# Kernel optimization log

Hardware: AMD Instinct MI355X
Metric: run time of the kernel (lower is better)

## Reference

```python
import jax, jax.numpy as jnp
import numpy as np

N_NODES = 100000
N_EDGES = 1600000
N_GRAPHS = 512
NEG_SLOPE = 0.2  # PyG GATConv default


def setup_inputs() -> dict:
    key = jax.random.key(0)
    ks = jax.random.split(key, 12)
    x = jax.random.normal(ks[0], (N_NODES, 75), dtype=jnp.float32)
    edge_index = jax.random.randint(ks[1], (2, N_EDGES), 0, N_NODES, dtype=jnp.int64 if jax.config.jax_enable_x64 else jnp.int32)
    batch = jnp.sort(jax.random.randint(ks[2], (N_NODES,), 0, N_GRAPHS, dtype=jnp.int32))
    s = lambda k, shp, fan: jax.random.normal(k, shp, dtype=jnp.float32) * (1.0 / np.sqrt(fan))
    return {
        "x": x, "edge_index": edge_index, "batch": batch,
        "W1": s(ks[3], (75, 64), 75),           # conv1: heads=8, out=8
        "att_src1": s(ks[4], (8, 8), 8),
        "att_dst1": s(ks[5], (8, 8), 8),
        "bias1": jnp.zeros((64,), jnp.float32),
        "W2": s(ks[6], (64, 128), 64),          # conv2: heads=1, out=128
        "att_src2": s(ks[7], (1, 128), 128),
        "att_dst2": s(ks[8], (1, 128), 128),
        "bias2": jnp.zeros((128,), jnp.float32),
        "Wg": s(ks[9], (128, 1), 128),
        "bg": jnp.zeros((1,), jnp.float32),
    }


def _gat_conv(x, src, dst, W, att_src, att_dst, bias, heads, out_ch):
    # x: [N, F_in]; edges src->dst (self-loops already included)
    n = x.shape[0]
    h = (x @ W).reshape(n, heads, out_ch)            # [N, H, C]
    a_src = (h * att_src).sum(-1)                    # [N, H]
    a_dst = (h * att_dst).sum(-1)                    # [N, H]
    e = a_src[src] + a_dst[dst]                      # [E, H]
    e = jax.nn.leaky_relu(e, NEG_SLOPE)
    # segment softmax over incoming edges of each dst node
    emax = jax.ops.segment_max(e, dst, num_segments=n)      # [N, H]
    ee = jnp.exp(e - emax[dst])
    denom = jax.ops.segment_sum(ee, dst, num_segments=n)    # [N, H]
    alpha = ee / denom[dst]                                  # [E, H]
    msg = h[src] * alpha[:, :, None]                          # [E, H, C]
    out = jax.ops.segment_sum(msg, dst, num_segments=n)      # [N, H, C]
    return out.reshape(n, heads * out_ch) + bias


def reference(x, edge_index, batch, W1, att_src1, att_dst1, bias1,
              W2, att_src2, att_dst2, bias2, Wg, bg):
    n = x.shape[0]
    # PyG GATConv adds self-loops by default
    loops = jnp.arange(n, dtype=edge_index.dtype)
    src = jnp.concatenate([edge_index[0], loops])
    dst = jnp.concatenate([edge_index[1], loops])
    # eval mode: dropout is identity
    x2 = jax.nn.elu(_gat_conv(x, src, dst, W1, att_src1, att_dst1, bias1, heads=8, out_ch=8))
    x4 = _gat_conv(x2, src, dst, W2, att_src2, att_dst2, bias2, heads=1, out_ch=128)
    y = jax.ops.segment_sum(x4, batch, num_segments=N_GRAPHS)  # global_add_pool
    return y @ Wg + bg  # [N_GRAPHS, 1]
```

## Files before the change

kernel.cpp:

```cpp
#include <hip/hip_runtime.h>
#include <hip/hip_bf16.h>
#include <math.h>

#define N_NODES 100000
#define N_EDGES 1600000
#define ET (N_EDGES + N_NODES)
#define N_GRAPHS 512
#define NEG_SLOPE 0.2f
#define G2_BLOCKS 1280

#define BSH 7
#define NDB 128
#define NBUCK ((N_NODES + NDB - 1) / NDB)
#define BCAP 2560
#define ABLK 512
#define CHUNK ((ET + ABLK - 1) / ABLK)
#define F1_OFF (ABLK + 3)
#define PRE_GRID (F1_OFF + 1536)

__device__ __forceinline__ void atomAddF(float* p, float v) { unsafeAtomicAdd(p, v); }
__device__ __forceinline__ float lrelu(float v) { return v >= 0.f ? v : NEG_SLOPE * v; }

__device__ __forceinline__ unsigned short f2bf(float f) {
    unsigned int u = __float_as_uint(f);
    u += 0x7FFFu + ((u >> 16) & 1u);
    return (unsigned short)(u >> 16);
}
__device__ __forceinline__ float bf2f(unsigned short s) { return __uint_as_float(((unsigned int)s) << 16); }
__device__ __forceinline__ float bflo(unsigned int p) { return __uint_as_float(p << 16); }
__device__ __forceinline__ float bfhi(unsigned int p) { return __uint_as_float(p & 0xFFFF0000u); }

__global__ __launch_bounds__(256) void k_pre(
    const int* __restrict__ ei, uint2* __restrict__ gbuf, int* __restrict__ bcur,
    const float* __restrict__ x, const float* __restrict__ W1,
    const float* __restrict__ as1, const float* __restrict__ ad1,
    const float* __restrict__ W2, const float* __restrict__ as2,
    const float* __restrict__ ad2, const float* __restrict__ Wg,
    const float* __restrict__ b2, const float* __restrict__ bg,
    unsigned short* __restrict__ h1p, unsigned short* __restrict__ a1sh,
    float* __restrict__ a1d, float* __restrict__ wv, float* __restrict__ out)
{
    __shared__ __align__(16) char smem[CHUNK * 8 + NBUCK * 16 + 1024];
    const int t = threadIdx.x;
    const int blk = blockIdx.x;

    if (blk >= ABLK && blk < F1_OFF) {
        const int bb = blk - ABLK;
        if (bb == 0) {
            if (t < 192) {
                int c = t & 63, which = t >> 6;
                const float* v = (which == 0) ? Wg : ((which == 1) ? as2 : ad2);
                float s = 0.f;
                #pragma unroll
                for (int k = 0; k < 128; ++k) s += W2[c * 128 + k] * v[k];
                wv[which * 64 + c] = s;
            } else if (t == 192) {
                float s = 0.f;
                #pragma unroll
                for (int k = 0; k < 128; ++k) s += b2[k] * Wg[k];
                wv[192] = s;
            }
        } else {
            int i = (bb - 1) * 256 + t;
            if (i < N_GRAPHS) out[i] = bg[0];
        }
        return;
    }

    if (blk >= F1_OFF) {
        float (*xs)[76] = (float (*)[76])smem;
        const int g = t >> 6;
        const int c = t & 63;
        const int vb = blk - F1_OFF;
        const int fstride = PRE_GRID - F1_OFF;
        for (int nb = vb; nb < N_NODES / 4; nb += fstride) {
            const int n = nb * 4 + g;
            const float* xr = x + (long)n * 75;
            xs[g][c] = xr[c];
            if (c < 11) xs[g][64 + c] = xr[64 + c];
            __syncthreads();
            float h = 0.f;
            #pragma unroll
            for (int k = 0; k < 75; ++k) h += xs[g][k] * W1[k * 64 + c];
            h1p[(long)n * 64 + c] = f2bf(h);
            const int head = c >> 3, lane = c & 7;
            float vs = h * as1[c];
            float vd = h * ad1[c];
            #pragma unroll
            for (int off = 1; off < 8; off <<= 1) {
                vs += __shfl_xor(vs, off, 64);
                vd += __shfl_xor(vd, off, 64);
            }
            if (lane == 0) { a1sh[n * 8 + head] = f2bf(vs); a1d[n * 8 + head] = vd; }
            __syncthreads();
        }
        return;
    }

    uint2* pairs = (uint2*)smem;
    int* hist  = (int*)(smem + CHUNK * 8);
    int* excl  = hist + NBUCK;
    int* gbase = excl + NBUCK;
    int* cnt2  = gbase + NBUCK;
    int* red   = cnt2 + NBUCK;
    const long e0 = (long)blk * CHUNK;
    const int  n  = (int)((e0 + CHUNK <= ET) ? CHUNK : (ET - e0));
    for (int i = t; i < NBUCK; i += 256) { hist[i] = 0; cnt2[i] = 0; }
    __syncthreads();
    for (int i = t; i < n; i += 256) {
        long e = e0 + i;
        int dst = (e < N_EDGES) ? ei[N_EDGES + e] : (int)(e - N_EDGES);
        atomicAdd(&hist[dst >> BSH], 1);
    }
    __syncthreads();
    {
        int lk[4]; int s = 0;
        #pragma unroll
        for (int k = 0; k < 4; ++k) {
            int idx = t * 4 + k;
            int v = (idx < NBUCK) ? hist[idx] : 0;
            lk[k] = s; s += v;
        }
        red[t] = s;
        __syncthreads();
        for (int off = 1; off < 256; off <<= 1) {
            int a = (t >= off) ? red[t - off] : 0;
            __syncthreads();
            red[t] += a;
            __syncthreads();
        }
        int p = red[t] - s;
        #pragma unroll
        for (int k = 0; k < 4; ++k) {
            int idx = t * 4 + k;
            if (idx < NBUCK) excl[idx] = p + lk[k];
        }
    }
    __syncthreads();
    for (int i = t; i < n; i += 256) {
        long e = e0 + i;
        int src, dst;
        if (e < N_EDGES) { src = ei[e]; dst = ei[N_EDGES + e]; }
        else             { src = dst = (int)(e - N_EDGES); }
        int b = dst >> BSH;
        int pos = excl[b] + atomicAdd(&cnt2[b], 1);
        pairs[pos] = make_uint2((unsigned)src, (unsigned)dst);
    }
    __syncthreads();
    for (int b = t; b < NBUCK; b += 256)
        gbase[b] = hist[b] ? atomicAdd(&bcur[b], hist[b]) : 0;
    __syncthreads();
    for (int i = t; i < n; i += 256) {
        uint2 pr = pairs[i];
        int b = (int)(pr.y >> BSH);
        gbuf[(long)b * BCAP + gbase[b] + (i - excl[b])] = pr;
    }
}

__global__ __launch_bounds__(512) void k_gat1(
    const uint2* __restrict__ gbuf, const int* __restrict__ bcur,
    int* __restrict__ rowptr, int* __restrict__ ecol,
    const unsigned short* __restrict__ a1sh, const float* __restrict__ a1d,
    const unsigned short* __restrict__ h1p, const float* __restrict__ bias1,
    const float* __restrict__ wv,
    float2* __restrict__ sg2, float* __restrict__ a2dv)
{
    __shared__ int lds_ecol[BCAP];
    __shared__ int hist[NDB], excl[NDB + 1], cnt2[NDB];
    __shared__ int red[512];
    const int t = threadIdx.x;
    const int b = blockIdx.x;
    const int d0 = b << BSH;
    const int nloc = (N_NODES - d0 < NDB) ? (N_NODES - d0) : NDB;
    const int cnt = bcur[b];

    int partial = 0;
    for (int i = t; i < b; i += 512) partial += bcur[i];
    red[t] = partial;
    __syncthreads();
    for (int off = 256; off > 0; off >>= 1) {
        if (t < off) red[t] += red[t + off];
        __syncthreads();
    }
    const int base = red[0];
    __syncthreads();

    if (t < NDB) { hist[t] = 0; cnt2[t] = 0; }
    __syncthreads();
    const uint2* eb = gbuf + (long)b * BCAP;
    for (int i = t; i < cnt; i += 512) atomicAdd(&hist[(int)eb[i].y - d0], 1);
    __syncthreads();
    {
        int v = (t < NDB) ? hist[t] : 0;
        if (t < NDB) red[t] = v;
        __syncthreads();
        for (int off = 1; off < NDB; off <<= 1) {
            int a = (t < NDB && t >= off) ? red[t - off] : 0;
            __syncthreads();
            if (t < NDB) red[t] += a;
            __syncthreads();
        }
        if (t < nloc) excl[t] = red[t] - v;
        if (t == 0) excl[nloc] = cnt;
    }
    __syncthreads();
    if (t < nloc) rowptr[d0 + t] = base + excl[t];
    if (b == NBUCK - 1 && t == 0) rowptr[N_NODES] = base + cnt;
    for (int i = t; i < cnt; i += 512) {
        uint2 pr = eb[i];
        int dl = (int)pr.y - d0;
        int slot = excl[dl] + atomicAdd(&cnt2[dl], 1);
        lds_ecol[slot] = (int)pr.x;
    }
    __syncthreads();
    for (int i = t; i < cnt; i += 512) ecol[base + i] = lds_ecol[i];

    const int wave = t >> 6;
    const int lane = t & 63;
    const int g = lane >> 3;
    const int l = lane & 7;
    for (int di = wave; di < nloc; di += 8) {
        const int dst = d0 + di;
        const int beg = excl[di], end = excl[di + 1];
        const float adh = a1d[(long)dst * 8 + l];

        float acc[8] = {0.f,0.f,0.f,0.f,0.f,0.f,0.f,0.f};
        float den = 0.f;

        int j = beg + g;
        bool v = (j < end);
        int s = v ? lds_ecol[j] : 0;
        unsigned short ab = a1sh[(long)s * 8 + l];
        uint4 pv = *(const uint4*)(h1p + (long)s * 64 + l * 8);

        for (int j0 = beg; j0 < end; j0 += 8) {
            int jn = j + 8;
            bool vn = (jn < end);
            int sn = vn ? lds_ecol[jn] : 0;
            unsigned short abn = a1sh[(long)sn * 8 + l];
            uint4 pvn = *(const uint4*)(h1p + (long)sn * 64 + l * 8);
            float ee = v ? __expf(lrelu(bf2f(ab) + adh)) : 0.f;
            den += ee;
            acc[0] += ee * bflo(pv.x); acc[1] += ee * bfhi(pv.x);
            acc[2] += ee * bflo(pv.y); acc[3] += ee * bfhi(pv.y);
            acc[4] += ee * bflo(pv.z); acc[5] += ee * bfhi(pv.z);
            acc[6] += ee * bflo(pv.w); acc[7] += ee * bfhi(pv.w);
            j = jn; v = vn; s = sn; ab = abn; pv = pvn;
        }
        #pragma unroll
        for (int off = 8; off <= 32; off <<= 1) {
            den += __shfl_xor(den, off, 64);
            #pragma unroll
            for (int k = 0; k < 8; ++k) acc[k] += __shfl_xor(acc[k], off, 64);
        }

        if (g == 0) {
            const float inv = 1.f / den;
            float pg = 0.f, ps = 0.f, pd = 0.f;
            #pragma unroll
            for (int k = 0; k < 8; ++k) {
                float vv = acc[k] * inv + bias1[l * 8 + k];
                vv = vv > 0.f ? vv : (__expf(vv) - 1.f);
                pg += vv * wv[l * 8 + k];
                ps += vv * wv[64 + l * 8 + k];
                pd += vv * wv[128 + l * 8 + k];
            }
            #pragma unroll
            for (int off = 1; off < 8; off <<= 1) {
                pg += __shfl_xor(pg, off, 64);
                ps += __shfl_xor(ps, off, 64);
                pd += __shfl_xor(pd, off, 64);
            }
            if (l == 0) { sg2[dst] = make_float2(ps, pg); a2dv[dst] = pd; }
        }
    }
}

__global__ __launch_bounds__(256) void k_gat2(
    const int* __restrict__ rowptr, const int* __restrict__ ecol,
    const float2* __restrict__ sg2, const float* __restrict__ a2dv,
    const float* __restrict__ wv, const int* __restrict__ batch,
    float* __restrict__ out)
{
    const int lane = threadIdx.x & 63;
    const int sl = lane & 15;
    const int sgid = ((blockIdx.x * 256 + threadIdx.x) >> 4);
    const int NS = G2_BLOCKS * 16;
    const int per = (N_NODES + NS - 1) / NS;
    const int n0 = sgid * per;
    const int n1 = min(n0 + per, N_NODES);
    const float bc = wv[192];

    float accg = 0.f;
    int curg = -1;
    for (int n = n0; n < n1; ++n) {
        const int beg = rowptr[n], end = rowptr[n + 1];
        const float adv = a2dv[n];
        float num = 0.f, den = 0.f;
        for (int j = beg + sl; j < end; j += 16) {
            int s = ecol[j];
            float2 v = sg2[s];
            float ee = __expf(lrelu(v.x + adv));
            den += ee;
            num += ee * v.y;
        }
        #pragma unroll
        for (int off = 1; off < 16; off <<= 1) {
            den += __shfl_xor(den, off, 64);
            num += __shfl_xor(num, off, 64);
        }
        if (sl == 0) {
            int gr = batch[n];
            if (gr != curg) {
                if (curg >= 0) atomAddF(out + curg, accg);
                curg = gr; accg = 0.f;
            }
            accg += num / den + bc;
        }
    }
    if (sl == 0 && curg >= 0) atomAddF(out + curg, accg);
}

extern "C" void kernel_launch(void* const* d_in, const int* in_sizes, int n_in,
                              void* d_out, int out_size, void* d_ws, size_t ws_size,
                              hipStream_t stream) {
    (void)in_sizes; (void)n_in; (void)out_size; (void)ws_size;
    const float* x     = (const float*)d_in[0];
    const int*   ei    = (const int*)d_in[1];
    const int*   batch = (const int*)d_in[2];
    const float* W1    = (const float*)d_in[3];
    const float* as1   = (const float*)d_in[4];
    const float* ad1   = (const float*)d_in[5];
    const float* b1    = (const float*)d_in[6];
    const float* W2    = (const float*)d_in[7];
    const float* as2   = (const float*)d_in[8];
    const float* ad2   = (const float*)d_in[9];
    const float* b2    = (const float*)d_in[10];
    const float* Wg    = (const float*)d_in[11];
    const float* bg    = (const float*)d_in[12];
    float* out = (float*)d_out;

    const long N = N_NODES;
    char* p = (char*)d_ws;
    int* rowptr = (int*)p;              p += (N + 4)        * sizeof(int);
    int* bcur   = (int*)p;              p += 1024           * sizeof(int);
    int* ecol   = (int*)p;              p += (long)ET       * sizeof(int);
    uint2* gbuf = (uint2*)p;            p += (long)NBUCK * BCAP * sizeof(uint2);
    unsigned short* h1p  = (unsigned short*)p; p += N * 64  * sizeof(unsigned short);
    unsigned short* a1sh = (unsigned short*)p; p += N * 8   * sizeof(unsigned short);
    float* a1d  = (float*)p;            p += N * 8          * sizeof(float);
    float2* sg2 = (float2*)p;           p += N              * sizeof(float2);
    float* a2dv = (float*)p;            p += N              * sizeof(float);
    float* wv   = (float*)p;            p += 256            * sizeof(float);

    hipMemsetAsync(bcur, 0, NBUCK * sizeof(int), stream);
    k_pre <<<PRE_GRID, 256, 0, stream>>>(ei, gbuf, bcur, x, W1, as1, ad1,
                                         W2, as2, ad2, Wg, b2, bg,
                                         h1p, a1sh, a1d, wv, out);
    k_gat1<<<NBUCK, 512, 0, stream>>>(gbuf, bcur, rowptr, ecol,
                                      a1sh, a1d, h1p, b1, wv, sg2, a2dv);
    k_gat2<<<G2_BLOCKS, 256, 0, stream>>>(rowptr, ecol, sg2, a2dv, wv, batch, out);
}
```

Before: 284.9 us.

## Assign one 8-lane group per destination node in GAT layer 1 with triple-buffered gathers

```diff
diff --git a/kernel.cpp b/kernel.cpp
--- a/kernel.cpp
+++ b/kernel.cpp
@@ -165,14 +165,15 @@
     const float* __restrict__ wv,
     float2* __restrict__ sg2, float* __restrict__ a2dv)
 {
-    __shared__ int lds_ecol[BCAP];
+    __shared__ int lds_src[BCAP];
     __shared__ int hist[NDB], excl[NDB + 1], cnt2[NDB];
     __shared__ int red[512];
     const int t = threadIdx.x;
     const int b = blockIdx.x;
     const int d0 = b << BSH;
     const int nloc = (N_NODES - d0 < NDB) ? (N_NODES - d0) : NDB;
-    const int cnt = bcur[b];
+    int cntr = bcur[b];
+    const int cnt = cntr < BCAP ? cntr : BCAP;
 
     int partial = 0;
     for (int i = t; i < b; i += 512) partial += bcur[i];
@@ -210,69 +211,86 @@
         uint2 pr = eb[i];
         int dl = (int)pr.y - d0;
         int slot = excl[dl] + atomicAdd(&cnt2[dl], 1);
-        lds_ecol[slot] = (int)pr.x;
-    }
-    __syncthreads();
-    for (int i = t; i < cnt; i += 512) ecol[base + i] = lds_ecol[i];
-
-    const int wave = t >> 6;
-    const int lane = t & 63;
-    const int g = lane >> 3;
-    const int l = lane & 7;
-    for (int di = wave; di < nloc; di += 8) {
-        const int dst = d0 + di;
-        const int beg = excl[di], end = excl[di + 1];
+        lds_src[slot] = (int)pr.x;
+    }
+    __syncthreads();
+    for (int i = t; i < cnt; i += 512) ecol[base + i] = lds_src[i];
+
+    const int l = t & 7;
+    const int gid = t >> 3;
+    for (int dl = gid; dl < nloc; dl += 64) {
+        const int dst = d0 + dl;
+        const int beg = excl[dl];
+        const int dgl = excl[dl + 1] - beg;
         const float adh = a1d[(long)dst * 8 + l];
 
         float acc[8] = {0.f,0.f,0.f,0.f,0.f,0.f,0.f,0.f};
         float den = 0.f;
 
-        int j = beg + g;
-        bool v = (j < end);
-        int s = v ? lds_ecol[j] : 0;
-        unsigned short ab = a1sh[(long)s * 8 + l];
-        uint4 pv = *(const uint4*)(h1p + (long)s * 64 + l * 8);
-
-        for (int j0 = beg; j0 < end; j0 += 8) {
-            int jn = j + 8;
-            bool vn = (jn < end);
-            int sn = vn ? lds_ecol[jn] : 0;
-            unsigned short abn = a1sh[(long)sn * 8 + l];
-            uint4 pvn = *(const uint4*)(h1p + (long)sn * 64 + l * 8);
-            float ee = v ? __expf(lrelu(bf2f(ab) + adh)) : 0.f;
+        bool v0 = true, v1 = 1 < dgl, v2 = 2 < dgl;
+        int s0 = lds_src[beg];
+        int s1 = v1 ? lds_src[beg + 1] : 0;
+        int s2 = v2 ? lds_src[beg + 2] : 0;
+        unsigned short ab0 = a1sh[(long)s0 * 8 + l];
+        unsigned short ab1 = a1sh[(long)s1 * 8 + l];
+        unsigned short ab2 = a1sh[(long)s2 * 8 + l];
+        uint4 pv0 = *(const uint4*)(h1p + (long)s0 * 64 + l * 8);
+        uint4 pv1 = *(const uint4*)(h1p + (long)s1 * 64 + l * 8);
+        uint4 pv2 = *(const uint4*)(h1p + (long)s2 * 64 + l * 8);
+
+        for (int j = 0; j < dgl; j += 3) {
+            float ee;
+            ee = v0 ? __expf(lrelu(bf2f(ab0) + adh)) : 0.f;
             den += ee;
-            acc[0] += ee * bflo(pv.x); acc[1] += ee * bfhi(pv.x);
-            acc[2] += ee * bflo(pv.y); acc[3] += ee * bfhi(pv.y);
-            acc[4] += ee * bflo(pv.z); acc[5] += ee * bfhi(pv.z);
-            acc[6] += ee * bflo(pv.w); acc[7] += ee * bfhi(pv.w);
-            j = jn; v = vn; s = sn; ab = abn; pv = pvn;
-        }
-        #pragma unroll
-        for (int off = 8; off <= 32; off <<= 1) {
-            den += __shfl_xor(den, off, 64);
-            #pragma unroll
-            for (int k = 0; k < 8; ++k) acc[k] += __shfl_xor(acc[k], off, 64);
-        }
-
-        if (g == 0) {
-            const float inv = 1.f / den;
-            float pg = 0.f, ps = 0.f, pd = 0.f;
-            #pragma unroll
-            for (int k = 0; k < 8; ++k) {
-                float vv = acc[k] * inv + bias1[l * 8 + k];
-                vv = vv > 0.f ? vv : (__expf(vv) - 1.f);
-                pg += vv * wv[l * 8 + k];
-                ps += vv * wv[64 + l * 8 + k];
-                pd += vv * wv[128 + l * 8 + k];
-            }
-            #pragma unroll
-            for (int off = 1; off < 8; off <<= 1) {
-                pg += __shfl_xor(pg, off, 64);
-                ps += __shfl_xor(ps, off, 64);
-                pd += __shfl_xor(pd, off, 64);
-            }
-            if (l == 0) { sg2[dst] = make_float2(ps, pg); a2dv[dst] = pd; }
-        }
+            acc[0] += ee * bflo(pv0.x); acc[1] += ee * bfhi(pv0.x);
+            acc[2] += ee * bflo(pv0.y); acc[3] += ee * bfhi(pv0.y);
+            acc[4] += ee * bflo(pv0.z); acc[5] += ee * bfhi(pv0.z);
+            acc[6] += ee * bflo(pv0.w); acc[7] += ee * bfhi(pv0.w);
+            v0 = (j + 3) < dgl;
+            int sn = v0 ? lds_src[beg + j + 3] : 0;
+            ab0 = a1sh[(long)sn * 8 + l];
+            pv0 = *(const uint4*)(h1p + (long)sn * 64 + l * 8);
+
+            ee = v1 ? __expf(lrelu(bf2f(ab1) + adh)) : 0.f;
+            den += ee;
+            acc[0] += ee * bflo(pv1.x); acc[1] += ee * bfhi(pv1.x);
+            acc[2] += ee * bflo(pv1.y); acc[3] += ee * bfhi(pv1.y);
+            acc[4] += ee * bflo(pv1.z); acc[5] += ee * bfhi(pv1.z);
+            acc[6] += ee * bflo(pv1.w); acc[7] += ee * bfhi(pv1.w);
+            v1 = (j + 4) < dgl;
+            sn = v1 ? lds_src[beg + j + 4] : 0;
+            ab1 = a1sh[(long)sn * 8 + l];
+            pv1 = *(const uint4*)(h1p + (long)sn * 64 + l * 8);
+
+            ee = v2 ? __expf(lrelu(bf2f(ab2) + adh)) : 0.f;
+            den += ee;
+            acc[0] += ee * bflo(pv2.x); acc[1] += ee * bfhi(pv2.x);
+            acc[2] += ee * bflo(pv2.y); acc[3] += ee * bfhi(pv2.y);
+            acc[4] += ee * bflo(pv2.z); acc[5] += ee * bfhi(pv2.z);
+            acc[6] += ee * bflo(pv2.w); acc[7] += ee * bfhi(pv2.w);
+            v2 = (j + 5) < dgl;
+            sn = v2 ? lds_src[beg + j + 5] : 0;
+            ab2 = a1sh[(long)sn * 8 + l];
+            pv2 = *(const uint4*)(h1p + (long)sn * 64 + l * 8);
+        }
+
+        const float inv = 1.f / den;
+        float pg = 0.f, ps = 0.f, pd = 0.f;
+        #pragma unroll
+        for (int k = 0; k < 8; ++k) {
+            float vv = acc[k] * inv + bias1[l * 8 + k];
+            vv = vv > 0.f ? vv : (__expf(vv) - 1.f);
+            pg += vv * wv[l * 8 + k];
+            ps += vv * wv[64 + l * 8 + k];
+            pd += vv * wv[128 + l * 8 + k];
+        }
+        #pragma unroll
+        for (int off = 1; off < 8; off <<= 1) {
+            pg += __shfl_xor(pg, off, 64);
+            ps += __shfl_xor(ps, off, 64);
+            pd += __shfl_xor(pd, off, 64);
+        }
+        if (l == 0) { sg2[dst] = make_float2(ps, pg); a2dv[dst] = pd; }
     }
 }
 
@@ -282,8 +300,7 @@
     const float* __restrict__ wv, const int* __restrict__ batch,
     float* __restrict__ out)
 {
-    const int lane = threadIdx.x & 63;
-    const int sl = lane & 15;
+    const int sl = threadIdx.x & 15;
     const int sgid = ((blockIdx.x * 256 + threadIdx.x) >> 4);
     const int NS = G2_BLOCKS * 16;
     const int per = (N_NODES + NS - 1) / NS;
```

After: 259.4 us. 9.0% less time.
